# Optimization experiments

Hardware: AMD Instinct MI355X
Metric: run time of the kernel (lower is better)

Reference implementation:

```python
import jax, jax.numpy as jnp
import numpy as np

LRELU_SLOPE = 0.01  # torch nn.LeakyReLU default


def _lrelu(v):
    return jnp.where(v > 0, v, LRELU_SLOPE * v)


def setup_inputs() -> dict:
    key = jax.random.key(0)
    ks = jax.random.split(key, 9)
    B, C, T = 16, 1024, 1500
    nbins, hid, emb = 4096, 512, 256
    s = 0.02
    return {
        "feature": jax.random.normal(ks[0], (B, C, T), jnp.float32),
        "centroid": jax.random.normal(ks[1], (nbins, C), jnp.float32),
        "ew0": jax.random.normal(ks[2], (hid, C), jnp.float32) * s,
        "eb0": jnp.zeros((hid,), jnp.float32),
        "ew1": jax.random.normal(ks[3], (hid, hid), jnp.float32) * s,
        "eb1": jnp.zeros((hid,), jnp.float32),
        "ew2": jax.random.normal(ks[4], (emb, hid), jnp.float32) * s,
        "eb2": jnp.zeros((emb,), jnp.float32),
        "dw0": jax.random.normal(ks[5], (hid, emb), jnp.float32) * s,
        "db0": jnp.zeros((hid,), jnp.float32),
        "dw1": jax.random.normal(ks[6], (hid, hid), jnp.float32) * s,
        "db1": jnp.zeros((hid,), jnp.float32),
        "dw2": jax.random.normal(ks[7], (C, hid), jnp.float32) * s,
        "db2": jnp.zeros((C,), jnp.float32),
    }


def reference(feature, centroid, ew0, eb0, ew1, eb1, ew2, eb2,
              dw0, db0, dw1, db1, dw2, db2):
    B, C, T = feature.shape
    # --- nearest-centroid match: squared-norm expansion + matmul + argmin ---
    x = feature.transpose(0, 2, 1).reshape(-1, C)          # (B*T, C)
    c_norm = jnp.sum(centroid * centroid, axis=1)          # (nbins,)
    dist = (jnp.sum(x * x, axis=1, keepdims=True)
            - 2.0 * (x @ centroid.T)
            + c_norm[None, :])                             # (B*T, nbins)
    idx = jnp.argmin(dist, axis=1)                         # (B*T,)
    lin_dec = centroid[idx].reshape(B, T, C).transpose(0, 2, 1)  # (B, C, T)
    # --- speaker residual + refiner autoencoder (quantizer = identity) ---
    spk_raw = feature - lin_dec                            # (B, C, T)
    h = spk_raw.transpose(0, 2, 1)                         # (B, T, C)
    h = _lrelu(h @ ew0.T + eb0)
    h = _lrelu(h @ ew1.T + eb1)
    z = h @ ew2.T + eb2                                    # (B, T, emb)
    h = _lrelu(z @ dw0.T + db0)
    h = _lrelu(h @ dw1.T + db1)
    spk_dec = (h @ dw2.T + db2).transpose(0, 2, 1)         # (B, C, T)
    return lin_dec + spk_dec
```

## Files before the change

### kernel.cpp

```cpp
#include <hip/hip_runtime.h>


typedef unsigned short u16;
typedef unsigned int   u32;
typedef __bf16 bf16x8 __attribute__((ext_vector_type(8)));
typedef float  f32x4  __attribute__((ext_vector_type(4)));

#define AS1 __attribute__((address_space(1)))
#define AS3 __attribute__((address_space(3)))

__device__ __forceinline__ u16 rne_bf16(float f) {
  u32 u = __float_as_uint(f);
  u = (u + 0x7FFFu + ((u >> 16) & 1u)) >> 16;
  return (u16)u;
}
__device__ __forceinline__ float b2f(u16 h) {
  return __uint_as_float(((u32)h) << 16);
}


__global__ __launch_bounds__(256) void conv_centroid(
    const float* __restrict__ cent, u16* __restrict__ chi, u16* __restrict__ clo,
    float* __restrict__ cnorm, int K)
{
  int row  = blockIdx.x * 4 + (threadIdx.x >> 6);
  int lane = threadIdx.x & 63;
  const float* cr = cent + (size_t)row * K;
  float s = 0.f;
  for (int j = 0; j < K; j += 64) {
    int k = j + lane;
    float f = cr[k];
    s += f * f;
    u32 u = __float_as_uint(f);
    u32 hi = (u + 0x7FFFu + ((u >> 16) & 1u)) >> 16;
    float fhi = __uint_as_float(hi << 16);
    chi[(size_t)row * K + k] = (u16)hi;
    clo[(size_t)row * K + k] = rne_bf16(f - fhi);
  }
#pragma unroll
  for (int m = 1; m < 64; m <<= 1) s += __shfl_xor(s, m, 64);
  if (lane == 0) cnorm[row] = s;
}

__global__ __launch_bounds__(256) void conv_feature(
    const float* __restrict__ feat, u16* __restrict__ xhi, u16* __restrict__ xlo,
    int C, int T)
{
  __shared__ float tile[64][65];
  int bb = blockIdx.z, c0 = blockIdx.y * 64, t0 = blockIdx.x * 64;
  const float* fb = feat + (size_t)bb * C * T;
#pragma unroll
  for (int i = 0; i < 16; ++i) {
    int id = threadIdx.x + i * 256;
    int lc = id >> 6, lt = id & 63;
    int t = t0 + lt;
    tile[lc][lt] = (t < T) ? fb[(size_t)(c0 + lc) * T + t] : 0.f;
  }
  __syncthreads();
#pragma unroll
  for (int i = 0; i < 16; ++i) {
    int id = threadIdx.x + i * 256;
    int lt = id >> 6, lc = id & 63;
    int t = t0 + lt;
    if (t < T) {
      size_t row = (size_t)bb * T + t;
      float f = tile[lc][lt];
      u32 u = __float_as_uint(f);
      u32 hi = (u + 0x7FFFu + ((u >> 16) & 1u)) >> 16;
      float fhi = __uint_as_float(hi << 16);
      xhi[row * C + c0 + lc] = (u16)hi;
      xlo[row * C + c0 + lc] = rne_bf16(f - fhi);
    }
  }
}

__global__ __launch_bounds__(256) void f2bf(
    const float* __restrict__ s, u16* __restrict__ d, int n)
{
  int i = blockIdx.x * 256 + threadIdx.x;
  if (i < n) d[i] = rne_bf16(s[i]);
}


template<int KK, int NSEG>
__global__ __launch_bounds__(512, 2) void score256(
    const u16* __restrict__ A0, const u16* __restrict__ A1, const u16* __restrict__ A2,
    const u16* __restrict__ B0s, const u16* __restrict__ B1s, const u16* __restrict__ B2s,
    const float* __restrict__ cnb, float* __restrict__ pval, int* __restrict__ pidx,
    int M, int N)
{
  constexpr int NKTPS = KK / 64;
  constexpr int NKT   = NSEG * NKTPS;
  static_assert(NKT % 2 == 0, "even tile count");

  __shared__ f32x4 smem4[8192];
  char* smem = (char*)smem4;

  const int lane = threadIdx.x & 63;
  const int wid  = threadIdx.x >> 6;
  const int wr   = wid >> 2;
  const int wc   = wid & 3;

  const int rowBase = blockIdx.y * 256;
  const int colBase = blockIdx.x * 256;

  const int kswz  = ((lane & 7) ^ (lane >> 3)) << 4;
  const int kbase = (lane >> 4) << 4;

  const f32x4 zero4 = {0.f, 0.f, 0.f, 0.f};
  f32x4 acc[8][4];
#pragma unroll
  for (int i = 0; i < 8; ++i)
#pragma unroll
    for (int j = 0; j < 4; ++j) acc[i][j] = zero4;

  bf16x8 aR[2][4][2];
  bf16x8 bR[2][2][2];

  auto stage = [&](int b, int isB, int h, int t) {
    int tc  = t < NKT ? t : NKT - 1;
    int seg = tc / NKTPS;
    int k0  = (tc - seg * NKTPS) << 6;
    const u16* S = isB ? (seg == 0 ? B0s : (seg == 1 ? B1s : B2s))
                       : (seg == 0 ? A0  : (seg == 1 ? A1  : A2));
    int rcBase = isB ? colBase : rowBase;
    char* dst = smem + (isB ? 65536 : 0) + b * 32768 + h * 16384 + wid * 1024;
#pragma unroll
    for (int j = 0; j < 2; ++j) {
      int r  = h * 128 + j * 64 + wid * 8 + (lane >> 3);
      int gr = rcBase + r;
      if (!isB) gr = gr < M ? gr : M - 1;
      const char* ga = (const char*)S + ((size_t)gr * KK + k0) * 2 + kswz;
      __builtin_amdgcn_global_load_lds((const AS1 void*)ga,
                                       (AS3 void*)(dst + j * 8192), 16, 0, 0);
    }
  };

#define LDA_H(b, qm) do { \
  _Pragma("unroll") for (int mf = 0; mf < 4; ++mf) { \
    int row = wr * 128 + (qm) * 64 + mf * 16 + (lane & 15); \
    const char* p = smem + (b) * 32768 + row * 128; \
    int sw = (row & 7) << 4; \
    aR[qm][mf][0] = *(const bf16x8*)(p + (kbase ^ sw)); \
    aR[qm][mf][1] = *(const bf16x8*)(p + ((kbase + 64) ^ sw)); \
  } } while (0)

#define LDB_H(b, qn) do { \
  _Pragma("unroll") for (int nf = 0; nf < 2; ++nf) { \
    int row = wc * 64 + (qn) * 32 + nf * 16 + (lane & 15); \
    const char* p = smem + 65536 + (b) * 32768 + row * 128; \
    int sw = (row & 7) << 4; \
    bR[qn][nf][0] = *(const bf16x8*)(p + (kbase ^ sw)); \
    bR[qn][nf][1] = *(const bf16x8*)(p + ((kbase + 64) ^ sw)); \
  } } while (0)

#define MMQ(qm, qn) do { \
  _Pragma("unroll") for (int mf = 0; mf < 4; ++mf) \
  _Pragma("unroll") for (int nf = 0; nf < 2; ++nf) { \
    acc[(qm)*4+mf][(qn)*2+nf] = __builtin_amdgcn_mfma_f32_16x16x32_bf16( \
        aR[qm][mf][0], bR[qn][nf][0], acc[(qm)*4+mf][(qn)*2+nf], 0, 0, 0); \
    acc[(qm)*4+mf][(qn)*2+nf] = __builtin_amdgcn_mfma_f32_16x16x32_bf16( \
        aR[qm][mf][1], bR[qn][nf][1], acc[(qm)*4+mf][(qn)*2+nf], 0, 0, 0); \
  } } while (0)

#define BAR()    __builtin_amdgcn_s_barrier()
#define PRIO1()  __builtin_amdgcn_s_setprio(1)
#define PRIO0()  __builtin_amdgcn_s_setprio(0)
#define VMCNT4() asm volatile("s_waitcnt vmcnt(4)" ::: "memory")

  stage(0, 0, 0, 0); stage(0, 0, 1, 0); stage(0, 1, 0, 0); stage(0, 1, 1, 0);
  stage(1, 0, 0, 1); stage(1, 0, 1, 1);
  VMCNT4();
  BAR();

  for (int i = 0; i < NKT / 2; ++i) {
    const int t = 2 * i;
    LDA_H(0, 0); LDB_H(0, 0);
    stage(1, 1, 0, t + 1);
    BAR(); PRIO1(); MMQ(0, 0); PRIO0(); BAR();
    LDB_H(0, 1); LDA_H(0, 1);
    stage(1, 1, 1, t + 1);
    BAR(); PRIO1(); MMQ(0, 1); PRIO0(); BAR();
    stage(0, 0, 0, t + 2);
    BAR(); PRIO1(); MMQ(1, 1); PRIO0(); BAR();
    stage(0, 0, 1, t + 2);
    BAR(); PRIO1(); MMQ(1, 0); PRIO0(); VMCNT4(); BAR();
    LDA_H(1, 0); LDB_H(1, 0);
    stage(0, 1, 0, t + 2);
    BAR(); PRIO1(); MMQ(0, 0); PRIO0(); BAR();
    LDB_H(1, 1); LDA_H(1, 1);
    stage(0, 1, 1, t + 2);
    BAR(); PRIO1(); MMQ(0, 1); PRIO0(); BAR();
    stage(1, 0, 0, t + 3);
    BAR(); PRIO1(); MMQ(1, 1); PRIO0(); BAR();
    stage(1, 0, 1, t + 3);
    BAR(); PRIO1(); MMQ(1, 0); PRIO0(); VMCNT4(); BAR();
  }

  const int colL = colBase + wc * 64 + (lane & 15);
  float cn[4];
#pragma unroll
  for (int ni = 0; ni < 4; ++ni) cn[ni] = 0.5f * cnb[colL + ni * 16];
  const int nchunk = N >> 6;
  const int chunk  = (colBase >> 6) + wc;
#pragma unroll
  for (int mi = 0; mi < 8; ++mi) {
#pragma unroll
    for (int reg = 0; reg < 4; ++reg) {
      float best = acc[mi][0][reg] - cn[0];
      int   bc   = colL;
#pragma unroll
      for (int ni = 1; ni < 4; ++ni) {
        float v  = acc[mi][ni][reg] - cn[ni];
        int   c2 = colL + ni * 16;
        if (v > best || (v == best && c2 < bc)) { best = v; bc = c2; }
      }
#pragma unroll
      for (int m = 1; m < 16; m <<= 1) {
        float vo = __shfl_xor(best, m, 64);
        int   co = __shfl_xor(bc,   m, 64);
        if (vo > best || (vo == best && co < bc)) { best = vo; bc = co; }
      }
      if ((lane & 15) == 0) {
        int row = rowBase + wr * 128 + (mi >> 2) * 64 + (mi & 3) * 16
                + ((lane >> 4) << 2) + reg;
        if (row < M) {
          pval[(size_t)row * nchunk + chunk] = best;
          pidx[(size_t)row * nchunk + chunk] = bc;
        }
      }
    }
  }
#undef LDA_H
#undef LDB_H
#undef MMQ
#undef BAR
#undef PRIO1
#undef PRIO0
#undef VMCNT4
}


template<int NSEG, bool SCORE, bool ACT>
__global__ __launch_bounds__(256) void gemm_bt(
    const u16* __restrict__ A0, const u16* __restrict__ A1, const u16* __restrict__ A2,
    const u16* __restrict__ B0, const u16* __restrict__ B1, const u16* __restrict__ B2,
    const float* __restrict__ cnb, u16* __restrict__ outb,
    float* __restrict__ pval, int* __restrict__ pidx,
    int M, int N, int K)
{
  __shared__ bf16x8 smem8[2048];
  char* smem = (char*)smem8;

  const int lane = threadIdx.x & 63;
  const int wid  = threadIdx.x >> 6;
  const int wm   = wid >> 1, wn = wid & 1;

  const int rowBase = blockIdx.y * 128;
  const int colBase = blockIdx.x * 128;

  const f32x4 zero4 = {0.f, 0.f, 0.f, 0.f};
  f32x4 acc[4][4];
#pragma unroll
  for (int i = 0; i < 4; ++i)
#pragma unroll
    for (int j = 0; j < 4; ++j) acc[i][j] = zero4;

  const int l8   = lane >> 3;
  const int kbsw = ((lane & 7) ^ l8) << 4;
  const int kseg = K >> 6;
  const int nkt  = NSEG * kseg;

  for (int kt = 0; kt < nkt; ++kt) {
    int seg, k0;
    if (NSEG == 1) { seg = 0; k0 = kt << 6; }
    else           { seg = kt / kseg; k0 = (kt - seg * kseg) << 6; }
    const u16* Aseg = (seg == 0) ? A0 : (seg == 1 ? A1 : A2);
    const u16* Bseg = (seg == 0) ? B0 : (seg == 1 ? B1 : B2);

#pragma unroll
    for (int i = 0; i < 4; ++i) {
      int c = wid * 4 + i;
      int r = c * 8 + l8;
      int gra = rowBase + r; gra = gra < M ? gra : (M - 1);
      const char* ga = (const char*)Aseg + ((size_t)gra * K + k0) * 2 + kbsw;
      __builtin_amdgcn_global_load_lds((const AS1 void*)ga,
                                       (AS3 void*)(smem + c * 1024), 16, 0, 0);
      int grb = colBase + r;
      const char* gb = (const char*)Bseg + ((size_t)grb * K + k0) * 2 + kbsw;
      __builtin_amdgcn_global_load_lds((const AS1 void*)gb,
                                       (AS3 void*)(smem + 16384 + c * 1024), 16, 0, 0);
    }
    __syncthreads();

#pragma unroll
    for (int kk = 0; kk < 64; kk += 32) {
      bf16x8 a[4], b[4];
      const int kb = (kk + ((lane >> 4) << 3)) << 1;
#pragma unroll
      for (int mf = 0; mf < 4; ++mf) {
        int row = wm * 64 + mf * 16 + (lane & 15);
        a[mf] = *(const bf16x8*)(smem + row * 128 + (kb ^ ((row & 7) << 4)));
      }
#pragma unroll
      for (int nf = 0; nf < 4; ++nf) {
        int row = wn * 64 + nf * 16 + (lane & 15);
        b[nf] = *(const bf16x8*)(smem + 16384 + row * 128 + (kb ^ ((row & 7) << 4)));
      }
#pragma unroll
      for (int mf = 0; mf < 4; ++mf)
#pragma unroll
        for (int nf = 0; nf < 4; ++nf)
          acc[mf][nf] = __builtin_amdgcn_mfma_f32_16x16x32_bf16(
              a[mf], b[nf], acc[mf][nf], 0, 0, 0);
    }
    __syncthreads();
  }

  const int colLane = colBase + wn * 64 + (lane & 15);

  if (SCORE) {
    float cn[4];
#pragma unroll
    for (int nf = 0; nf < 4; ++nf) cn[nf] = 0.5f * cnb[colLane + nf * 16];
    const int nchunk = N >> 6;
    const int chunk  = (colBase >> 6) + wn;
#pragma unroll
    for (int mf = 0; mf < 4; ++mf) {
#pragma unroll
      for (int reg = 0; reg < 4; ++reg) {
        float best = acc[mf][0][reg] - cn[0];
        int   bc   = colLane;
#pragma unroll
        for (int nf = 1; nf < 4; ++nf) {
          float v = acc[mf][nf][reg] - cn[nf];
          int c2 = colLane + nf * 16;
          if (v > best || (v == best && c2 < bc)) { best = v; bc = c2; }
        }
#pragma unroll
        for (int m = 1; m < 16; m <<= 1) {
          float vo = __shfl_xor(best, m, 64);
          int   co = __shfl_xor(bc,   m, 64);
          if (vo > best || (vo == best && co < bc)) { best = vo; bc = co; }
        }
        if ((lane & 15) == 0) {
          int row = rowBase + wm * 64 + mf * 16 + ((lane >> 4) << 2) + reg;
          if (row < M) {
            pval[(size_t)row * nchunk + chunk] = best;
            pidx[(size_t)row * nchunk + chunk] = bc;
          }
        }
      }
    }
  } else {
    float bl[4];
#pragma unroll
    for (int nf = 0; nf < 4; ++nf) bl[nf] = cnb[colLane + nf * 16];
#pragma unroll
    for (int mf = 0; mf < 4; ++mf)
#pragma unroll
      for (int nf = 0; nf < 4; ++nf)
#pragma unroll
        for (int reg = 0; reg < 4; ++reg) {
          int row = rowBase + wm * 64 + mf * 16 + ((lane >> 4) << 2) + reg;
          if (row < M) {
            float v = acc[mf][nf][reg] + bl[nf];
            if (ACT) v = v > 0.f ? v : 0.01f * v;
            outb[(size_t)row * N + colLane + nf * 16] = rne_bf16(v);
          }
        }
  }
}


__global__ __launch_bounds__(256) void argmax_reduce(
    const float* __restrict__ pval, const int* __restrict__ pidx,
    int* __restrict__ idxOut, int nchunk)
{
  int row  = blockIdx.x * 4 + (threadIdx.x >> 6);
  int lane = threadIdx.x & 63;
  float v = pval[(size_t)row * nchunk + lane];
  int   c = pidx[(size_t)row * nchunk + lane];
#pragma unroll
  for (int m = 1; m < 64; m <<= 1) {
    float vo = __shfl_xor(v, m, 64);
    int   co = __shfl_xor(c, m, 64);
    if (vo > v || (vo == v && co < c)) { v = vo; c = co; }
  }
  if (lane == 0) idxOut[row] = c;
}

__global__ __launch_bounds__(256) void build_spk(
    const u16* __restrict__ xhi, const u16* __restrict__ xlo,
    const float* __restrict__ cent, const int* __restrict__ idx,
    u16* __restrict__ spk, int C)
{
  int row = blockIdx.x;
  const float* cr = cent + (size_t)idx[row] * C;
  size_t base = (size_t)row * C;
  for (int c = threadIdx.x; c < C; c += 256) {
    float v = b2f(xhi[base + c]) + b2f(xlo[base + c]) - cr[c];
    spk[base + c] = rne_bf16(v);
  }
}

__global__ __launch_bounds__(256) void transpose_out(
    const u16* __restrict__ spkdec, const float* __restrict__ cent,
    const int* __restrict__ idx, float* __restrict__ out, int C, int T)
{
  __shared__ float tile[64][65];
  int r0 = blockIdx.x * 64, c0 = blockIdx.y * 64;
#pragma unroll
  for (int i = 0; i < 16; ++i) {
    int id = threadIdx.x + i * 256;
    int lr = id >> 6, lc = id & 63;
    int row = r0 + lr;
    tile[lr][lc] = b2f(spkdec[(size_t)row * C + c0 + lc])
                 + cent[(size_t)idx[row] * C + c0 + lc];
  }
  __syncthreads();
#pragma unroll
  for (int i = 0; i < 16; ++i) {
    int id = threadIdx.x + i * 256;
    int lc = id >> 6, lr = id & 63;
    int row = r0 + lr;
    int b = row / T, t = row - b * T;
    out[((size_t)b * C + c0 + lc) * T + t] = tile[lr][lc];
  }
}


extern "C" void kernel_launch(void* const* d_in, const int* in_sizes, int n_in,
                              void* d_out, int out_size, void* d_ws, size_t ws_size,
                              hipStream_t stream)
{
  const float* feature  = (const float*)d_in[0];
  const float* centroid = (const float*)d_in[1];
  const float* ew0 = (const float*)d_in[2];
  const float* eb0 = (const float*)d_in[3];
  const float* ew1 = (const float*)d_in[4];
  const float* eb1 = (const float*)d_in[5];
  const float* ew2 = (const float*)d_in[6];
  const float* eb2 = (const float*)d_in[7];
  const float* dw0 = (const float*)d_in[8];
  const float* db0 = (const float*)d_in[9];
  const float* dw1 = (const float*)d_in[10];
  const float* db1 = (const float*)d_in[11];
  const float* dw2 = (const float*)d_in[12];
  const float* db2 = (const float*)d_in[13];
  float* out = (float*)d_out;

  const int Bb = 16, C = 1024, T = 1500, M = Bb * T;
  const int NBIN = 4096, HID = 512, EMB = 256;
  const int MB  = (M + 127) / 128;
  const int MB2 = (M + 255) / 256;

  char* ws = (char*)d_ws;
  size_t off = 0;
  auto alloc = [&](size_t bytes) -> char* {
    char* p = ws + off;
    off += (bytes + 255) & ~(size_t)255;
    return p;
  };
  u16*   c_hi  = (u16*)  alloc((size_t)NBIN * C * 2);
  u16*   c_lo  = (u16*)  alloc((size_t)NBIN * C * 2);
  float* cnorm = (float*)alloc((size_t)NBIN * 4);
  u16*   wb0   = (u16*)  alloc((size_t)HID * C   * 2);
  u16*   wb1   = (u16*)  alloc((size_t)HID * HID * 2);
  u16*   wb2   = (u16*)  alloc((size_t)EMB * HID * 2);
  u16*   wb3   = (u16*)  alloc((size_t)HID * EMB * 2);
  u16*   wb4   = (u16*)  alloc((size_t)HID * HID * 2);
  u16*   wb5   = (u16*)  alloc((size_t)C   * HID * 2);
  u16*   x_hi  = (u16*)  alloc((size_t)M * C * 2);
  u16*   x_lo  = (u16*)  alloc((size_t)M * C * 2);
  int*   idx   = (int*)  alloc((size_t)M * 4);
  char*  spkR  =         alloc((size_t)M * C * 2);
  u16*   spk   = (u16*)spkR;
  float* pval  = (float*)spkR;
  int*   pidx  = (int*)(spkR + (size_t)M * 64 * 4);
  u16*   h1    = (u16*)  alloc((size_t)M * HID * 2);
  u16*   h2    = (u16*)  alloc((size_t)M * HID * 2);
  u16*   hz    = (u16*)  alloc((size_t)M * EMB * 2);

  conv_centroid<<<NBIN / 4, 256, 0, stream>>>(centroid, c_hi, c_lo, cnorm, C);
  conv_feature<<<dim3((T + 63) / 64, C / 64, Bb), 256, 0, stream>>>(feature, x_hi, x_lo, C, T);
  f2bf<<<(HID * C   + 255) / 256, 256, 0, stream>>>(ew0, wb0, HID * C);
  f2bf<<<(HID * HID + 255) / 256, 256, 0, stream>>>(ew1, wb1, HID * HID);
  f2bf<<<(EMB * HID + 255) / 256, 256, 0, stream>>>(ew2, wb2, EMB * HID);
  f2bf<<<(HID * EMB + 255) / 256, 256, 0, stream>>>(dw0, wb3, HID * EMB);
  f2bf<<<(HID * HID + 255) / 256, 256, 0, stream>>>(dw1, wb4, HID * HID);
  f2bf<<<(C   * HID + 255) / 256, 256, 0, stream>>>(dw2, wb5, C * HID);

  score256<1024, 3><<<dim3(NBIN / 256, MB2), 512, 0, stream>>>(
      x_hi, x_lo, x_hi, c_hi, c_hi, c_lo, cnorm, pval, pidx, M, NBIN);

  argmax_reduce<<<M / 4, 256, 0, stream>>>(pval, pidx, idx, NBIN / 64);
  build_spk<<<M, 256, 0, stream>>>(x_hi, x_lo, centroid, idx, spk, C);

  gemm_bt<1, false, true ><<<dim3(HID / 128, MB), 256, 0, stream>>>(
      spk, spk, spk, wb0, wb0, wb0, eb0, h1, nullptr, nullptr, M, HID, C);
  gemm_bt<1, false, true ><<<dim3(HID / 128, MB), 256, 0, stream>>>(
      h1, h1, h1, wb1, wb1, wb1, eb1, h2, nullptr, nullptr, M, HID, HID);
  gemm_bt<1, false, false><<<dim3(EMB / 128, MB), 256, 0, stream>>>(
      h2, h2, h2, wb2, wb2, wb2, eb2, hz, nullptr, nullptr, M, EMB, HID);
  gemm_bt<1, false, true ><<<dim3(HID / 128, MB), 256, 0, stream>>>(
      hz, hz, hz, wb3, wb3, wb3, db0, h1, nullptr, nullptr, M, HID, EMB);
  gemm_bt<1, false, true ><<<dim3(HID / 128, MB), 256, 0, stream>>>(
      h1, h1, h1, wb4, wb4, wb4, db1, h2, nullptr, nullptr, M, HID, HID);
  gemm_bt<1, false, false><<<dim3(C / 128, MB), 256, 0, stream>>>(
      h2, h2, h2, wb5, wb5, wb5, db2, spk, nullptr, nullptr, M, C, HID);

  transpose_out<<<dim3(M / 64, C / 64), 256, 0, stream>>>(spk, centroid, idx, out, C, T);
}
```

Baseline: 1.086 ms.

## Reschedule centroid GEMM pipeline with split A/B staging and explicit LDS waits

Splits the global-to-LDS staging helper into separate A and B loaders and reorders the ping-pong schedule so B tiles are prefetched ahead and A tiles are staged later. The A fragment register buffer shrinks from two quarter-sets to one, and A fragments are reloaded just before the MFMA quarter that needs them. Explicit lgkmcnt waits plus scheduling barriers are placed before each MFMA block so the compiler cannot hoist math above outstanding LDS reads. The intent is lower register pressure and better overlap of LDS reads, global loads and MFMA. The cost is extra LDS reads and serialising waits that may stall the matrix pipes.

Measured after the change: 1.016 ms. -6.5%, faster.

```diff
diff --git a/kernel.cpp b/kernel.cpp
--- a/kernel.cpp
+++ b/kernel.cpp
@@ -114,38 +114,50 @@
 #pragma unroll
     for (int j = 0; j < 4; ++j) acc[i][j] = zero4;
 
-  bf16x8 aR[2][4][2];
+  bf16x8 aR[4][2];
   bf16x8 bR[2][2][2];
 
-  auto stage = [&](int b, int isB, int h, int t) {
+  auto stageA = [&](int b, int h, int t) {
     int tc  = t < NKT ? t : NKT - 1;
     int seg = tc / NKTPS;
     int k0  = (tc - seg * NKTPS) << 6;
-    const u16* S = isB ? (seg == 0 ? B0s : (seg == 1 ? B1s : B2s))
-                       : (seg == 0 ? A0  : (seg == 1 ? A1  : A2));
-    int rcBase = isB ? colBase : rowBase;
-    char* dst = smem + (isB ? 65536 : 0) + b * 32768 + h * 16384 + wid * 1024;
+    const u16* S = (seg == 0 ? A0 : (seg == 1 ? A1 : A2));
+    char* dst = smem + b * 32768 + h * 16384 + wid * 1024;
 #pragma unroll
     for (int j = 0; j < 2; ++j) {
       int r  = h * 128 + j * 64 + wid * 8 + (lane >> 3);
-      int gr = rcBase + r;
-      if (!isB) gr = gr < M ? gr : M - 1;
+      int gr = rowBase + r; gr = gr < M ? gr : M - 1;
       const char* ga = (const char*)S + ((size_t)gr * KK + k0) * 2 + kswz;
       __builtin_amdgcn_global_load_lds((const AS1 void*)ga,
                                        (AS3 void*)(dst + j * 8192), 16, 0, 0);
     }
   };
-
-#define LDA_H(b, qm) do { \
+  auto stageB = [&](int b, int h, int t) {
+    int tc  = t < NKT ? t : NKT - 1;
+    int seg = tc / NKTPS;
+    int k0  = (tc - seg * NKTPS) << 6;
+    const u16* S = (seg == 0 ? B0s : (seg == 1 ? B1s : B2s));
+    char* dst = smem + 65536 + b * 32768 + h * 16384 + wid * 1024;
+#pragma unroll
+    for (int j = 0; j < 2; ++j) {
+      int r  = h * 128 + j * 64 + wid * 8 + (lane >> 3);
+      int gr = colBase + r;
+      const char* ga = (const char*)S + ((size_t)gr * KK + k0) * 2 + kswz;
+      __builtin_amdgcn_global_load_lds((const AS1 void*)ga,
+                                       (AS3 void*)(dst + j * 8192), 16, 0, 0);
+    }
+  };
+
+#define LDA_Q(b, qm) do { \
   _Pragma("unroll") for (int mf = 0; mf < 4; ++mf) { \
     int row = wr * 128 + (qm) * 64 + mf * 16 + (lane & 15); \
     const char* p = smem + (b) * 32768 + row * 128; \
     int sw = (row & 7) << 4; \
-    aR[qm][mf][0] = *(const bf16x8*)(p + (kbase ^ sw)); \
-    aR[qm][mf][1] = *(const bf16x8*)(p + ((kbase + 64) ^ sw)); \
+    aR[mf][0] = *(const bf16x8*)(p + (kbase ^ sw)); \
+    aR[mf][1] = *(const bf16x8*)(p + ((kbase + 64) ^ sw)); \
   } } while (0)
 
-#define LDB_H(b, qn) do { \
+#define LDB_Q(b, qn) do { \
   _Pragma("unroll") for (int nf = 0; nf < 2; ++nf) { \
     int row = wc * 64 + (qn) * 32 + nf * 16 + (lane & 15); \
     const char* p = smem + 65536 + (b) * 32768 + row * 128; \
@@ -158,43 +170,52 @@
   _Pragma("unroll") for (int mf = 0; mf < 4; ++mf) \
   _Pragma("unroll") for (int nf = 0; nf < 2; ++nf) { \
     acc[(qm)*4+mf][(qn)*2+nf] = __builtin_amdgcn_mfma_f32_16x16x32_bf16( \
-        aR[qm][mf][0], bR[qn][nf][0], acc[(qm)*4+mf][(qn)*2+nf], 0, 0, 0); \
+        aR[mf][0], bR[qn][nf][0], acc[(qm)*4+mf][(qn)*2+nf], 0, 0, 0); \
     acc[(qm)*4+mf][(qn)*2+nf] = __builtin_amdgcn_mfma_f32_16x16x32_bf16( \
-        aR[qm][mf][1], bR[qn][nf][1], acc[(qm)*4+mf][(qn)*2+nf], 0, 0, 0); \
+        aR[mf][1], bR[qn][nf][1], acc[(qm)*4+mf][(qn)*2+nf], 0, 0, 0); \
   } } while (0)
 
-#define BAR()    __builtin_amdgcn_s_barrier()
-#define PRIO1()  __builtin_amdgcn_s_setprio(1)
-#define PRIO0()  __builtin_amdgcn_s_setprio(0)
-#define VMCNT4() asm volatile("s_waitcnt vmcnt(4)" ::: "memory")
-
-  stage(0, 0, 0, 0); stage(0, 0, 1, 0); stage(0, 1, 0, 0); stage(0, 1, 1, 0);
-  stage(1, 0, 0, 1); stage(1, 0, 1, 1);
+#define BAR()     __builtin_amdgcn_s_barrier()
+#define PRIO1()   __builtin_amdgcn_s_setprio(1)
+#define PRIO0()   __builtin_amdgcn_s_setprio(0)
+#define VMCNT4()  asm volatile("s_waitcnt vmcnt(4)" ::: "memory")
+#define LGKM8()   asm volatile("s_waitcnt lgkmcnt(8)" ::: "memory")
+#define LGKM0_SB() do { asm volatile("s_waitcnt lgkmcnt(0)" ::: "memory"); \
+                        __builtin_amdgcn_sched_barrier(0); } while (0)
+
+  stageA(0, 0, 0); stageA(0, 1, 0); stageB(0, 0, 0); stageB(0, 1, 0);
+  stageB(1, 0, 1); stageB(1, 1, 1);
   VMCNT4();
   BAR();
 
   for (int i = 0; i < NKT / 2; ++i) {
     const int t = 2 * i;
-    LDA_H(0, 0); LDB_H(0, 0);
-    stage(1, 1, 0, t + 1);
-    BAR(); PRIO1(); MMQ(0, 0); PRIO0(); BAR();
-    LDB_H(0, 1); LDA_H(0, 1);
-    stage(1, 1, 1, t + 1);
-    BAR(); PRIO1(); MMQ(0, 1); PRIO0(); BAR();
-    stage(0, 0, 0, t + 2);
-    BAR(); PRIO1(); MMQ(1, 1); PRIO0(); BAR();
-    stage(0, 0, 1, t + 2);
-    BAR(); PRIO1(); MMQ(1, 0); PRIO0(); VMCNT4(); BAR();
-    LDA_H(1, 0); LDB_H(1, 0);
-    stage(0, 1, 0, t + 2);
-    BAR(); PRIO1(); MMQ(0, 0); PRIO0(); BAR();
-    LDB_H(1, 1); LDA_H(1, 1);
-    stage(0, 1, 1, t + 2);
-    BAR(); PRIO1(); MMQ(0, 1); PRIO0(); BAR();
-    stage(1, 0, 0, t + 3);
-    BAR(); PRIO1(); MMQ(1, 1); PRIO0(); BAR();
-    stage(1, 0, 1, t + 3);
-    BAR(); PRIO1(); MMQ(1, 0); PRIO0(); VMCNT4(); BAR();
+    LDA_Q(0, 0); LDB_Q(0, 0);
+    stageA(1, 0, t + 1);
+    LGKM8();
+    BAR(); LGKM0_SB(); PRIO1(); MMQ(0, 0); PRIO0(); BAR();
+    LDB_Q(0, 1);
+    stageA(1, 1, t + 1);
+    BAR(); LGKM0_SB(); PRIO1(); MMQ(0, 1); PRIO0(); BAR();
+    LDA_Q(0, 1);
+    stageB(0, 0, t + 2);
+    BAR(); LGKM0_SB(); PRIO1(); MMQ(1, 1); PRIO0(); BAR();
+    stageB(0, 1, t + 2);
+    VMCNT4();
+    BAR(); PRIO1(); MMQ(1, 0); PRIO0(); BAR();
+    LDA_Q(1, 0); LDB_Q(1, 0);
+    stageA(0, 0, t + 2);
+    LGKM8();
+    BAR(); LGKM0_SB(); PRIO1(); MMQ(0, 0); PRIO0(); BAR();
+    LDB_Q(1, 1);
+    stageA(0, 1, t + 2);
+    BAR(); LGKM0_SB(); PRIO1(); MMQ(0, 1); PRIO0(); BAR();
+    LDA_Q(1, 1);
+    stageB(1, 0, t + 3);
+    BAR(); LGKM0_SB(); PRIO1(); MMQ(1, 1); PRIO0(); BAR();
+    stageB(1, 1, t + 3);
+    VMCNT4();
+    BAR(); PRIO1(); MMQ(1, 0); PRIO0(); BAR();
   }
 
   const int colL = colBase + wc * 64 + (lane & 15);
@@ -231,13 +252,15 @@
       }
     }
   }
-#undef LDA_H
-#undef LDB_H
+#undef LDA_Q
+#undef LDB_Q
 #undef MMQ
 #undef BAR
 #undef PRIO1
 #undef PRIO0
 #undef VMCNT4
+#undef LGKM8
+#undef LGKM0_SB
 }
 
 
```
